# Optimization experiments

Measured on AMD Instinct MI355X. Metric: run time of the kernel, lower is better.

The kernel has to match this reference:

```python
import jax, jax.numpy as jnp
import numpy as np

EPS = 1e-12
NUM_ITERATIONS = 3


def squash(t, axis=-1):
    sn = jnp.sum(t * t, axis=axis, keepdims=True)
    scale = sn / (1.0 + sn + EPS)
    return scale * t / jnp.sqrt(sn + EPS)


def setup_inputs() -> dict:
    key = jax.random.key(0)
    k1, k2 = jax.random.split(key)
    B, R, IN, OUT, C = 128, 4096, 16, 32, 2
    x = jax.random.normal(k1, (B, R, IN), dtype=jnp.float32)
    # learned parameter: torch.randn(num_capsules, num_route_nodes, in, out)
    route_weights = jax.random.normal(k2, (C, R, IN, OUT), dtype=jnp.float32)
    return {"x": x, "route_weights": route_weights}


def reference(x, route_weights):
    # priors: [C, B, R, 1, O] == x[None,:,:,None,:] @ W[:,None,:,:,:]
    priors = jnp.einsum('bri,crio->cbro', x, route_weights)[..., None, :]
    # logits kept [C,B,R,1,1]: the torch code stores [C,B,R,1,O] but every
    # update (delta_logits) is constant along O, so softmax over axis=2 is identical.
    logits = jnp.zeros(priors.shape[:-1] + (1,), dtype=priors.dtype)
    outputs = None
    for i in range(NUM_ITERATIONS):
        probs = jax.nn.softmax(logits, axis=2)                      # over route nodes
        s = jnp.sum(probs * priors, axis=2, keepdims=True)          # [C,B,1,1,O]
        outputs = squash(s, axis=-1)
        if i != NUM_ITERATIONS - 1:
            delta = jnp.sum(priors * outputs, axis=-1, keepdims=True)  # [C,B,R,1,1]
            logits = logits + delta
    return outputs
```

## Files before the change

kernel.cpp:

```cpp
#include <hip/hip_runtime.h>
#include <math.h>

#define CB    128
#define CR    4096
#define CIN   16
#define COUT  32
#define CCAP  2
#define RC    16
#define NRCH  (CR / RC)
#define EPSF  1e-12f

typedef _Float16 h8  __attribute__((ext_vector_type(8)));
typedef _Float16 h4t __attribute__((ext_vector_type(4)));
typedef float    f4  __attribute__((ext_vector_type(4)));
typedef float    f8v __attribute__((ext_vector_type(8)));

__device__ __forceinline__ void stage_pack_W(const float* __restrict__ w,
                                             int c, int r0, int t,
                                             _Float16* WpL, float* Stg)
{
  h4t* WpL4 = (h4t*)WpL;
#pragma unroll
  for (int h = 0; h < 2; ++h) {
    const float4* src = (const float4*)(w + ((size_t)c * CR + r0 + h * 8) * 512);
    ((float4*)Stg)[t]       = src[t];
    ((float4*)Stg)[t + 512] = src[t + 512];
    __syncthreads();
#pragma unroll
    for (int q = 0; q < 2; ++q) {
      const int sl  = t * 2 + q;
      const int rr  = sl >> 7;
      const int rem = sl & 127;
      const int ot  = rem >> 6;
      const int gs  = (rem >> 4) & 3;
      const int ms  = rem & 15;
      h4t v;
#pragma unroll
      for (int j = 0; j < 4; ++j)
        v[j] = (_Float16)Stg[rr * 512 + (4 * gs + j) * 32 + ot * 16 + ms];
      WpL4[(h * 8 + rr) * 128 + rem] = v;
    }
    __syncthreads();
  }
}

__device__ __forceinline__ void store_partials(float* __restrict__ partialA,
                                               float* __restrict__ partialE,
                                               const float* accA, const float* accB,
                                               float esum, int c, int rch,
                                               int t, int g, int b)
{
  float4 a4 = {accA[0], accA[1], accA[2], accA[3]};
  float4 b4 = {accB[0], accB[1], accB[2], accB[3]};
  float* dst = partialA + ((size_t)(c * NRCH + rch)) * 4096 + (size_t)t * 8;
  *(float4*)dst = a4;
  *(float4*)(dst + 4) = b4;
  if (g == 0) partialE[((size_t)(c * NRCH + rch)) * CB + b] = esum;
}

__global__ __launch_bounds__(512) void caps_pass0_kernel(
    const float* __restrict__ x, const float* __restrict__ w,
    h8* __restrict__ priors16,
    float* __restrict__ partialA, float* __restrict__ partialE)
{
  const int blk = (int)blockIdx.x;
  const int c = blk >> 8, rch = blk & 255;
  const int r0 = rch * RC;
  const int t = (int)threadIdx.x;
  const int wv = t >> 6, L = t & 63, g = L >> 4, m = L & 15;
  const int b  = wv * 16 + m;

  __shared__ __align__(16) char lds[32768];
  _Float16* WpL = (_Float16*)lds;
  float* Stg = (float*)(lds + 16384);

  stage_pack_W(w, c, r0, t, WpL, Stg);

  const h4t* WpL4 = (const h4t*)WpL;
  h8* prow = priors16 + ((size_t)(c * NRCH + rch)) * RC * 512 + t;

  float accA[4] = {0.f, 0.f, 0.f, 0.f};
  float accB[4] = {0.f, 0.f, 0.f, 0.f};

#pragma unroll 4
  for (int ri = 0; ri < RC; ++ri) {
    const int r = r0 + ri;
    float4 xf = *(const float4*)(x + ((size_t)b * CR + r) * CIN + 4 * g);
    h8 bx = {(_Float16)xf.x, (_Float16)xf.y, (_Float16)xf.z, (_Float16)xf.w,
             (_Float16)0.f, (_Float16)0.f, (_Float16)0.f, (_Float16)0.f};
    h4t wA4 = WpL4[ri * 128 + L];
    h4t wB4 = WpL4[ri * 128 + 64 + L];
    h8 aA = {wA4[0], wA4[1], wA4[2], wA4[3],
             (_Float16)0.f, (_Float16)0.f, (_Float16)0.f, (_Float16)0.f};
    h8 aB = {wB4[0], wB4[1], wB4[2], wB4[3],
             (_Float16)0.f, (_Float16)0.f, (_Float16)0.f, (_Float16)0.f};
    f4 z = {0.f, 0.f, 0.f, 0.f};
    f4 pA = __builtin_amdgcn_mfma_f32_16x16x32_f16(aA, bx, z, 0, 0, 0);
    f4 pB = __builtin_amdgcn_mfma_f32_16x16x32_f16(aB, bx, z, 0, 0, 0);

    h8 pk = {(_Float16)pA[0], (_Float16)pA[1], (_Float16)pA[2], (_Float16)pA[3],
             (_Float16)pB[0], (_Float16)pB[1], (_Float16)pB[2], (_Float16)pB[3]};
    prow[ri * 512] = pk;

#pragma unroll
    for (int j = 0; j < 4; ++j) { accA[j] += pA[j]; accB[j] += pB[j]; }
  }
  store_partials(partialA, partialE, accA, accB, (float)RC, 0 * 0 + c, rch, t, g, b);
}

__global__ __launch_bounds__(512) void caps_passN_kernel(
    const h8* __restrict__ priors16, const float* __restrict__ vsum,
    float* __restrict__ partialA, float* __restrict__ partialE)
{
  const int blk = (int)blockIdx.x;
  const int c = blk >> 8, rch = blk & 255;
  const int t = (int)threadIdx.x;
  const int wv = t >> 6, L = t & 63, g = L >> 4, m = L & 15;
  const int b  = wv * 16 + m;

  const float* vb = vsum + ((size_t)c * CB + b) * COUT;
  float4 vA = *(const float4*)(vb + 4 * g);
  float4 vB = *(const float4*)(vb + 16 + 4 * g);

  const h8* prow = priors16 + ((size_t)(c * NRCH + rch)) * RC * 512 + t;

  float accA[4] = {0.f, 0.f, 0.f, 0.f};
  float accB[4] = {0.f, 0.f, 0.f, 0.f};
  float esum = 0.f;

#pragma unroll 4
  for (int ri = 0; ri < RC; ++ri) {
    f8v p = __builtin_convertvector(prow[ri * 512], f8v);
    float d = p[0] * vA.x + p[1] * vA.y + p[2] * vA.z + p[3] * vA.w
            + p[4] * vB.x + p[5] * vB.y + p[6] * vB.z + p[7] * vB.w;
    d += __shfl_xor(d, 16);
    d += __shfl_xor(d, 32);
    const float e = __expf(d);
    esum += e;
#pragma unroll
    for (int j = 0; j < 4; ++j) { accA[j] += e * p[j]; accB[j] += e * p[4 + j]; }
  }
  store_partials(partialA, partialE, accA, accB, esum, c, rch, t, g, b);
}

__global__ __launch_bounds__(256) void caps_redv_kernel(
    const float* __restrict__ partialA, const float* __restrict__ partialE,
    float* __restrict__ vsum, float* __restrict__ out, int mode)
{
  const int cb = (int)blockIdx.x;
  const int c2 = cb >> 7, b2 = cb & 127;
  const int t  = (int)threadIdx.x;
  const int o = t & 31, jg = t >> 5;
  const int wv2 = b2 >> 4, m2 = b2 & 15;
  const int half = o >> 4, oo = o & 15, g2 = oo >> 2, j2 = oo & 3;
  const size_t idx = (size_t)(wv2 * 64 + g2 * 16 + m2) * 8 + half * 4 + j2;

  __shared__ float red[8][33];
  __shared__ float rede[8];

  float s = 0.f;
#pragma unroll 4
  for (int k = 0; k < NRCH / 8; ++k) {
    const int j = jg + k * 8;
    s += partialA[((size_t)(c2 * NRCH + j)) * 4096 + idx];
  }
  red[jg][o] = s;
  __syncthreads();

  if (t < 8) {
    float e = 0.f;
#pragma unroll 4
    for (int k = 0; k < NRCH / 8; ++k)
      e += partialE[((size_t)(c2 * NRCH + t + k * 8)) * CB + b2];
    rede[t] = e;
  }
  __syncthreads();

  if (t < 32) {
    float sv = 0.f, es = 0.f;
#pragma unroll
    for (int jj = 0; jj < 8; ++jj) { sv += red[jj][t]; es += rede[jj]; }
    float sm = sv / es;
    float sn = sm * sm;
#pragma unroll
    for (int sh = 1; sh < 32; sh <<= 1) sn += __shfl_xor(sn, sh);
    float fac = sn / ((1.f + sn + EPSF) * sqrtf(sn + EPSF));
    float vv = sm * fac;
    if (mode == 2)      out[cb * COUT + t]  = vv;
    else if (mode == 1) vsum[cb * COUT + t] += vv;
    else                vsum[cb * COUT + t] = vv;
  }
}

extern "C" void kernel_launch(void* const* d_in, const int* in_sizes, int n_in,
                              void* d_out, int out_size, void* d_ws, size_t ws_size,
                              hipStream_t stream) {
  const float* x = (const float*)d_in[0];
  const float* w = (const float*)d_in[1];
  float* out = (float*)d_out;

  char* p = (char*)d_ws;
  h8* priors16 = (h8*)p;
  p += (size_t)CCAP * NRCH * RC * 512 * sizeof(h8);
  float* vsum = (float*)p;
  p += (size_t)CCAP * CB * COUT * sizeof(float);
  float* partialA = (float*)p;
  p += (size_t)CCAP * NRCH * 4096 * sizeof(float);
  float* partialE = (float*)p;

  caps_pass0_kernel<<<dim3(CCAP * NRCH), 512, 0, stream>>>(
      x, w, priors16, partialA, partialE);
  caps_redv_kernel<<<dim3(CCAP * CB), 256, 0, stream>>>(
      partialA, partialE, vsum, out, 0);
  caps_passN_kernel<<<dim3(CCAP * NRCH), 512, 0, stream>>>(
      priors16, vsum, partialA, partialE);
  caps_redv_kernel<<<dim3(CCAP * CB), 256, 0, stream>>>(
      partialA, partialE, vsum, out, 1);
  caps_passN_kernel<<<dim3(CCAP * NRCH), 512, 0, stream>>>(
      priors16, vsum, partialA, partialE);
  caps_redv_kernel<<<dim3(CCAP * CB), 256, 0, stream>>>(
      partialA, partialE, vsum, out, 2);
}
```

Before: 79.71 us.

## Recompute priors via MFMA each pass instead of materializing fp16 priors

After: 78.77 us. About the same (-1.2%).

```diff
diff --git a/kernel.cpp b/kernel.cpp
--- a/kernel.cpp
+++ b/kernel.cpp
@@ -11,37 +11,34 @@
 #define EPSF  1e-12f
 
 typedef _Float16 h8  __attribute__((ext_vector_type(8)));
-typedef _Float16 h4t __attribute__((ext_vector_type(4)));
 typedef float    f4  __attribute__((ext_vector_type(4)));
-typedef float    f8v __attribute__((ext_vector_type(8)));
 
-__device__ __forceinline__ void stage_pack_W(const float* __restrict__ w,
-                                             int c, int r0, int t,
-                                             _Float16* WpL, float* Stg)
+__global__ __launch_bounds__(256) void caps_prepack_kernel(
+    const float* __restrict__ w, h8* __restrict__ wp)
 {
-  h4t* WpL4 = (h4t*)WpL;
+  const int blk = (int)blockIdx.x;
+  const int c   = blk >> 10;
+  const int r0  = (blk & 1023) * 4;
+  const int t   = (int)threadIdx.x;
+
+  __shared__ __align__(16) float Wl[4 * 512];
+  {
+    const float4* src = (const float4*)(w + ((size_t)c * CR + r0) * 512);
+    ((float4*)Wl)[t]       = src[t];
+    ((float4*)Wl)[t + 256] = src[t + 256];
+  }
+  __syncthreads();
+
+  const int rr = t >> 6;
+  const int L  = t & 63;
+  const int g  = L >> 4, m = L & 15;
+  h8 v;
 #pragma unroll
-  for (int h = 0; h < 2; ++h) {
-    const float4* src = (const float4*)(w + ((size_t)c * CR + r0 + h * 8) * 512);
-    ((float4*)Stg)[t]       = src[t];
-    ((float4*)Stg)[t + 512] = src[t + 512];
-    __syncthreads();
-#pragma unroll
-    for (int q = 0; q < 2; ++q) {
-      const int sl  = t * 2 + q;
-      const int rr  = sl >> 7;
-      const int rem = sl & 127;
-      const int ot  = rem >> 6;
-      const int gs  = (rem >> 4) & 3;
-      const int ms  = rem & 15;
-      h4t v;
-#pragma unroll
-      for (int j = 0; j < 4; ++j)
-        v[j] = (_Float16)Stg[rr * 512 + (4 * gs + j) * 32 + ot * 16 + ms];
-      WpL4[(h * 8 + rr) * 128 + rem] = v;
-    }
-    __syncthreads();
+  for (int j = 0; j < 4; ++j) {
+    v[j]     = (_Float16)Wl[rr * 512 + (4 * g + j) * 32 + m];
+    v[4 + j] = (_Float16)Wl[rr * 512 + (4 * g + j) * 32 + 16 + m];
   }
+  wp[((size_t)c * CR + r0 + rr) * 64 + L] = v;
 }
 
 __device__ __forceinline__ void store_partials(float* __restrict__ partialA,
@@ -58,10 +55,11 @@
   if (g == 0) partialE[((size_t)(c * NRCH + rch)) * CB + b] = esum;
 }
 
-__global__ __launch_bounds__(512) void caps_pass0_kernel(
-    const float* __restrict__ x, const float* __restrict__ w,
-    h8* __restrict__ priors16,
-    float* __restrict__ partialA, float* __restrict__ partialE)
+__global__ __launch_bounds__(512) void caps_pass_kernel(
+    const float* __restrict__ x, const h8* __restrict__ wp,
+    const float* __restrict__ vsum,
+    float* __restrict__ partialA, float* __restrict__ partialE,
+    int uniform)
 {
   const int blk = (int)blockIdx.x;
   const int c = blk >> 8, rch = blk & 255;
@@ -70,59 +68,15 @@
   const int wv = t >> 6, L = t & 63, g = L >> 4, m = L & 15;
   const int b  = wv * 16 + m;
 
-  __shared__ __align__(16) char lds[32768];
-  _Float16* WpL = (_Float16*)lds;
-  float* Stg = (float*)(lds + 16384);
+  const h8* wrow = wp + ((size_t)c * CR + r0) * 64 + L;
+  const float* xrow = x + ((size_t)b * CR + r0) * CIN + 4 * g;
 
-  stage_pack_W(w, c, r0, t, WpL, Stg);
-
-  const h4t* WpL4 = (const h4t*)WpL;
-  h8* prow = priors16 + ((size_t)(c * NRCH + rch)) * RC * 512 + t;
-
-  float accA[4] = {0.f, 0.f, 0.f, 0.f};
-  float accB[4] = {0.f, 0.f, 0.f, 0.f};
-
-#pragma unroll 4
-  for (int ri = 0; ri < RC; ++ri) {
-    const int r = r0 + ri;
-    float4 xf = *(const float4*)(x + ((size_t)b * CR + r) * CIN + 4 * g);
-    h8 bx = {(_Float16)xf.x, (_Float16)xf.y, (_Float16)xf.z, (_Float16)xf.w,
-             (_Float16)0.f, (_Float16)0.f, (_Float16)0.f, (_Float16)0.f};
-    h4t wA4 = WpL4[ri * 128 + L];
-    h4t wB4 = WpL4[ri * 128 + 64 + L];
-    h8 aA = {wA4[0], wA4[1], wA4[2], wA4[3],
-             (_Float16)0.f, (_Float16)0.f, (_Float16)0.f, (_Float16)0.f};
-    h8 aB = {wB4[0], wB4[1], wB4[2], wB4[3],
-             (_Float16)0.f, (_Float16)0.f, (_Float16)0.f, (_Float16)0.f};
-    f4 z = {0.f, 0.f, 0.f, 0.f};
-    f4 pA = __builtin_amdgcn_mfma_f32_16x16x32_f16(aA, bx, z, 0, 0, 0);
-    f4 pB = __builtin_amdgcn_mfma_f32_16x16x32_f16(aB, bx, z, 0, 0, 0);
-
-    h8 pk = {(_Float16)pA[0], (_Float16)pA[1], (_Float16)pA[2], (_Float16)pA[3],
-             (_Float16)pB[0], (_Float16)pB[1], (_Float16)pB[2], (_Float16)pB[3]};
-    prow[ri * 512] = pk;
-
-#pragma unroll
-    for (int j = 0; j < 4; ++j) { accA[j] += pA[j]; accB[j] += pB[j]; }
+  float4 vA = {0.f, 0.f, 0.f, 0.f}, vB = {0.f, 0.f, 0.f, 0.f};
+  if (!uniform) {
+    const float* vb = vsum + ((size_t)c * CB + b) * COUT;
+    vA = *(const float4*)(vb + 4 * g);
+    vB = *(const float4*)(vb + 16 + 4 * g);
   }
-  store_partials(partialA, partialE, accA, accB, (float)RC, 0 * 0 + c, rch, t, g, b);
-}
-
-__global__ __launch_bounds__(512) void caps_passN_kernel(
-    const h8* __restrict__ priors16, const float* __restrict__ vsum,
-    float* __restrict__ partialA, float* __restrict__ partialE)
-{
-  const int blk = (int)blockIdx.x;
-  const int c = blk >> 8, rch = blk & 255;
-  const int t = (int)threadIdx.x;
-  const int wv = t >> 6, L = t & 63, g = L >> 4, m = L & 15;
-  const int b  = wv * 16 + m;
-
-  const float* vb = vsum + ((size_t)c * CB + b) * COUT;
-  float4 vA = *(const float4*)(vb + 4 * g);
-  float4 vB = *(const float4*)(vb + 16 + 4 * g);
-
-  const h8* prow = priors16 + ((size_t)(c * NRCH + rch)) * RC * 512 + t;
 
   float accA[4] = {0.f, 0.f, 0.f, 0.f};
   float accB[4] = {0.f, 0.f, 0.f, 0.f};
@@ -130,15 +84,29 @@
 
 #pragma unroll 4
   for (int ri = 0; ri < RC; ++ri) {
-    f8v p = __builtin_convertvector(prow[ri * 512], f8v);
-    float d = p[0] * vA.x + p[1] * vA.y + p[2] * vA.z + p[3] * vA.w
-            + p[4] * vB.x + p[5] * vB.y + p[6] * vB.z + p[7] * vB.w;
-    d += __shfl_xor(d, 16);
-    d += __shfl_xor(d, 32);
-    const float e = __expf(d);
+    float4 xf = *(const float4*)(xrow + ri * CIN);
+    h8 bx = {(_Float16)xf.x, (_Float16)xf.y, (_Float16)xf.z, (_Float16)xf.w,
+             (_Float16)0.f, (_Float16)0.f, (_Float16)0.f, (_Float16)0.f};
+    h8 wf = wrow[ri * 64];
+    h8 aA = {wf[0], wf[1], wf[2], wf[3],
+             (_Float16)0.f, (_Float16)0.f, (_Float16)0.f, (_Float16)0.f};
+    h8 aB = {wf[4], wf[5], wf[6], wf[7],
+             (_Float16)0.f, (_Float16)0.f, (_Float16)0.f, (_Float16)0.f};
+    f4 z = {0.f, 0.f, 0.f, 0.f};
+    f4 pA = __builtin_amdgcn_mfma_f32_16x16x32_f16(aA, bx, z, 0, 0, 0);
+    f4 pB = __builtin_amdgcn_mfma_f32_16x16x32_f16(aB, bx, z, 0, 0, 0);
+
+    float e = 1.f;
+    if (!uniform) {
+      float d = pA[0] * vA.x + pA[1] * vA.y + pA[2] * vA.z + pA[3] * vA.w
+              + pB[0] * vB.x + pB[1] * vB.y + pB[2] * vB.z + pB[3] * vB.w;
+      d += __shfl_xor(d, 16);
+      d += __shfl_xor(d, 32);
+      e = __expf(d);
+    }
     esum += e;
 #pragma unroll
-    for (int j = 0; j < 4; ++j) { accA[j] += e * p[j]; accB[j] += e * p[4 + j]; }
+    for (int j = 0; j < 4; ++j) { accA[j] += e * pA[j]; accB[j] += e * pB[j]; }
   }
   store_partials(partialA, partialE, accA, accB, esum, c, rch, t, g, b);
 }
@@ -200,24 +168,25 @@
   float* out = (float*)d_out;
 
   char* p = (char*)d_ws;
-  h8* priors16 = (h8*)p;
-  p += (size_t)CCAP * NRCH * RC * 512 * sizeof(h8);
+  h8* wp = (h8*)p;
+  p += (size_t)CCAP * CR * 64 * sizeof(h8);
   float* vsum = (float*)p;
   p += (size_t)CCAP * CB * COUT * sizeof(float);
   float* partialA = (float*)p;
   p += (size_t)CCAP * NRCH * 4096 * sizeof(float);
   float* partialE = (float*)p;
 
-  caps_pass0_kernel<<<dim3(CCAP * NRCH), 512, 0, stream>>>(
-      x, w, priors16, partialA, partialE);
+  caps_prepack_kernel<<<dim3(CCAP * 1024), 256, 0, stream>>>(w, wp);
+  caps_pass_kernel<<<dim3(CCAP * NRCH), 512, 0, stream>>>(
+      x, wp, vsum, partialA, partialE, 1);
   caps_redv_kernel<<<dim3(CCAP * CB), 256, 0, stream>>>(
       partialA, partialE, vsum, out, 0);
-  caps_passN_kernel<<<dim3(CCAP * NRCH), 512, 0, stream>>>(
-      priors16, vsum, partialA, partialE);
+  caps_pass_kernel<<<dim3(CCAP * NRCH), 512, 0, stream>>>(
+      x, wp, vsum, partialA, partialE, 0);
   caps_redv_kernel<<<dim3(CCAP * CB), 256, 0, stream>>>(
       partialA, partialE, vsum, out, 1);
-  caps_passN_kernel<<<dim3(CCAP * NRCH), 512, 0, stream>>>(
-      priors16, vsum, partialA, partialE);
+  caps_pass_kernel<<<dim3(CCAP * NRCH), 512, 0, stream>>>(
+      x, wp, vsum, partialA, partialE, 0);
   caps_redv_kernel<<<dim3(CCAP * CB), 256, 0, stream>>>(
       partialA, partialE, vsum, out, 2);
 }
```
